# Optimization experiments

Hardware: AMD Instinct MI355X
Metric: run time of the kernel (lower is better)

Reference implementation:

```python
import jax, jax.numpy as jnp
import numpy as np

B, S, D, H = 4, 4096, 512, 512


def setup_inputs() -> dict:
    key = jax.random.key(0)
    ks = jax.random.split(key, 11)
    def rn(k, shape):
        return jax.random.normal(k, shape, dtype=jnp.float32)
    return {
        "query": rn(ks[0], (B, 1, D)),
        "keys": rn(ks[1], (B, S, D)),
        "values": rn(ks[2], (B, S, D)),
        "Wq": rn(ks[3], (D, H)) / np.sqrt(D),
        "bq": rn(ks[4], (H,)) * 0.02,
        "Wk": rn(ks[5], (D, H)) / np.sqrt(D),
        "bk": rn(ks[6], (H,)) * 0.02,
        "Wv": rn(ks[7], (D, H)) / np.sqrt(D),
        "bv": rn(ks[8], (H,)) * 0.02,
        "Wo": rn(ks[9], (H, D)) / np.sqrt(H),
        "bo": rn(ks[10], (D,)) * 0.02,
    }


def reference(query, keys, values, Wq, bq, Wk, bk, Wv, bv, Wo, bo):
    # projections
    q = query @ Wq + bq      # (B, 1, H)
    k = keys @ Wk + bk       # (B, S, H)
    v = values @ Wv + bv     # (B, S, H)
    scale = jnp.sqrt(jnp.asarray(q.shape[-1], dtype=jnp.float32))
    # single-query scores: (B, 1, S)
    scores = jnp.einsum('bqh,bsh->bqs', q, k)
    seq = k.shape[1]
    # torch masked_fill broadcasts (B,1,S) against tril (1,S,S) -> (B,S,S)
    causal = jnp.tril(jnp.ones((seq, seq), dtype=bool))[None]  # (1, S, S)
    masked = jnp.where(causal, scores, -jnp.inf)                # (B, S, S)
    attn_weights = jax.nn.softmax(masked / scale, axis=-1)      # (B, S, S)
    context = jnp.einsum('brs,bsh->brh', attn_weights, v)       # (B, S, H)
    out = context @ Wo + bo                                     # (B, S, D)
    return out, attn_weights
```

## Files before the change

kernel.cpp:

```cpp
#include <hip/hip_runtime.h>
#include <hip/hip_bf16.h>

#define BB 4
#define SS 4096
#define DD 512
#define HH 512

typedef __attribute__((ext_vector_type(8))) short bf16x8;
typedef __attribute__((ext_vector_type(4))) float f32x4;

__global__ __launch_bounds__(256) void k_pre1(const float* __restrict__ query,
                                              const float* __restrict__ Wq,
                                              const float* __restrict__ bq,
                                              const float* __restrict__ Wv,
                                              const float* __restrict__ Wo,
                                              float* __restrict__ qv,
                                              float* __restrict__ Wvop) {
    __shared__ float smem[8320];
    int wb = blockIdx.x, tid = threadIdx.x;
    if (wb < 32) {
        float* qs = smem;
        float (*red)[64] = reinterpret_cast<float(*)[64]>(smem + 512);
        int hg = wb & 7, b = wb >> 3;
        int hl = tid & 63, qq = tid >> 6;
        int h = hg * 64 + hl;
        for (int d = tid; d < DD; d += 256) qs[d] = query[b * DD + d];
        __syncthreads();
        float a = 0.f;
        int d0 = qq * 128;
        for (int d = d0; d < d0 + 128; ++d)
            a += qs[d] * Wq[(size_t)d * HH + h];
        red[qq][hl] = a;
        __syncthreads();
        if (tid < 64)
            qv[b * HH + hg * 64 + tid] = red[0][tid] + red[1][tid] + red[2][tid] + red[3][tid]
                                       + bq[hg * 64 + tid];
    } else {
        int t = wb - 32;
        int hs = t >> 6, rem = t & 63;
        int n0 = (rem & 7) * 64, k0 = (rem >> 3) * 64;
        float (*lo)[65] = reinterpret_cast<float(*)[65]>(smem);
        float (*lv)[65] = reinterpret_cast<float(*)[65]>(smem + 4160);
        int tn = (tid & 15) * 4, tk = (tid >> 4) * 4;
        float acc[4][4] = {};
        int hbase = hs * 128;
        for (int h0 = hbase; h0 < hbase + 128; h0 += 64) {
            for (int i = tid; i < 64 * 64; i += 256) {
                int rr = i >> 6, cc = i & 63;
                lo[rr][cc] = Wo[(size_t)(h0 + rr) * DD + n0 + cc];
                lv[rr][cc] = Wv[(size_t)(k0 + rr) * HH + h0 + cc];
            }
            __syncthreads();
            for (int h = 0; h < 64; ++h)
#pragma unroll
                for (int a = 0; a < 4; ++a) {
                    float vv = lv[tk + a][h];
#pragma unroll
                    for (int c = 0; c < 4; ++c) acc[a][c] += vv * lo[h][tn + c];
                }
            __syncthreads();
        }
        float* dst = Wvop + (size_t)hs * (DD * HH);
        for (int a = 0; a < 4; ++a)
            for (int c = 0; c < 4; ++c)
                dst[(size_t)(k0 + tk + a) * DD + n0 + tn + c] = acc[a][c];
    }
}

__global__ __launch_bounds__(256) void k_pre2(const float* __restrict__ Wk,
                                              const float* __restrict__ qv,
                                              const float* __restrict__ bk,
                                              const float* __restrict__ Wvop,
                                              const float* __restrict__ bv,
                                              const float* __restrict__ Wo,
                                              const float* __restrict__ bo,
                                              float* __restrict__ wout,
                                              float* __restrict__ cq,
                                              __hip_bfloat16* __restrict__ WvoT,
                                              float* __restrict__ bfinal) {
    __shared__ float smem[4160];
    int wb = blockIdx.x, tid = threadIdx.x;
    if (wb < 512) {
        float* qs = smem;
        float* red = smem + 512;
        int b = wb >> 7, dg = wb & 127;
        int wid = tid >> 6, lane = tid & 63;
        for (int h = tid; h < HH; h += 256) qs[h] = qv[b * HH + h];
        __syncthreads();
        int d = dg * 4 + wid;
        const float4* row = reinterpret_cast<const float4*>(Wk + (size_t)d * HH);
        float4 r0 = row[lane * 2], r1 = row[lane * 2 + 1];
        int h = lane * 8;
        float acc = r0.x * qs[h] + r0.y * qs[h + 1] + r0.z * qs[h + 2] + r0.w * qs[h + 3]
                  + r1.x * qs[h + 4] + r1.y * qs[h + 5] + r1.z * qs[h + 6] + r1.w * qs[h + 7];
        for (int off = 32; off > 0; off >>= 1) acc += __shfl_down(acc, off);
        if (lane == 0) wout[b * DD + d] = acc;
        if (dg == 0) {
            red[tid] = qs[tid] * bk[tid] + qs[tid + 256] * bk[tid + 256];
            __syncthreads();
            for (int off = 128; off > 0; off >>= 1) {
                if (tid < off) red[tid] += red[tid + off];
                __syncthreads();
            }
            if (tid == 0) cq[b] = red[0];
        }
    } else if (wb < 576) {
        int t = wb - 512;
        int n0 = (t & 7) * 64, k0 = (t >> 3) * 64;
        float (*ts)[65] = reinterpret_cast<float(*)[65]>(smem);
#pragma unroll
        for (int i = 0; i < 16; ++i) {
            int idx = tid + i * 256;
            int kk = idx >> 6, nn = idx & 63;
            size_t off = (size_t)(k0 + kk) * DD + n0 + nn;
            float s = Wvop[off] + Wvop[(size_t)DD * HH + off]
                    + Wvop[2 * (size_t)DD * HH + off] + Wvop[3 * (size_t)DD * HH + off];
            ts[nn][kk] = s;
        }
        __syncthreads();
#pragma unroll
        for (int i = 0; i < 16; ++i) {
            int idx = tid + i * 256;
            int row = idx >> 6, col = idx & 63;
            WvoT[(size_t)(n0 + row) * DD + k0 + col] = __float2bfloat16(ts[row][col]);
        }
    } else {
        int n0 = (wb - 576) * 64;
        int nn = tid & 63, hs = tid >> 6;
        float acc = 0.f;
        for (int hh = 0; hh < 128; ++hh) {
            int h = hs * 128 + hh;
            acc += bv[h] * Wo[(size_t)h * DD + n0 + nn];
        }
        float (*red)[64] = reinterpret_cast<float(*)[64]>(smem);
        red[hs][nn] = acc;
        __syncthreads();
        if (tid < 64)
            bfinal[n0 + tid] = red[0][tid] + red[1][tid] + red[2][tid] + red[3][tid]
                             + bo[n0 + tid];
    }
}

__global__ __launch_bounds__(256) void k_scores(const float* __restrict__ keys,
                                                const float* __restrict__ wv,
                                                const float* __restrict__ cq,
                                                float* __restrict__ scores) {
    __shared__ float ws[DD];
    int wb = blockIdx.x, tid = threadIdx.x;
    int b = wb >> 10, sg = wb & 1023;
    int wid = tid >> 6, lane = tid & 63;
    for (int d = tid; d < DD; d += 256) ws[d] = wv[b * DD + d];
    __syncthreads();
    int s = sg * 4 + wid;
    const float4* row = reinterpret_cast<const float4*>(keys + ((size_t)b * SS + s) * DD);
    float4 r0 = row[lane * 2], r1 = row[lane * 2 + 1];
    int h = lane * 8;
    float acc = r0.x * ws[h] + r0.y * ws[h + 1] + r0.z * ws[h + 2] + r0.w * ws[h + 3]
              + r1.x * ws[h + 4] + r1.y * ws[h + 5] + r1.z * ws[h + 6] + r1.w * ws[h + 7];
    for (int off = 32; off > 0; off >>= 1) acc += __shfl_down(acc, off);
    if (lane == 0) scores[b * SS + s] = acc + cq[b];
}

__global__ __launch_bounds__(1024) void k_softmax(const float* __restrict__ scores,
                                                  float* __restrict__ p,
                                                  float* __restrict__ inv_cum) {
    int b = blockIdx.x, tid = threadIdx.x;
    int wid = tid >> 6, lane = tid & 63;
    __shared__ float wmax[16];
    __shared__ float wsum[16];
    const float inv_scale = 0.04419417382415922f;
    float4 sv = *reinterpret_cast<const float4*>(scores + (size_t)b * SS + tid * 4);
    float loc[4] = {sv.x * inv_scale, sv.y * inv_scale, sv.z * inv_scale, sv.w * inv_scale};
    float mx = fmaxf(fmaxf(loc[0], loc[1]), fmaxf(loc[2], loc[3]));
    for (int off = 32; off > 0; off >>= 1) mx = fmaxf(mx, __shfl_xor(mx, off));
    if (lane == 0) wmax[wid] = mx;
    __syncthreads();
    float M = wmax[0];
    for (int i = 1; i < 16; ++i) M = fmaxf(M, wmax[i]);
    float own = 0.f;
    for (int j = 0; j < 4; ++j) {
        loc[j] = expf(loc[j] - M);
        own += loc[j];
    }
    float incl = own;
    for (int off = 1; off < 64; off <<= 1) {
        float v = __shfl_up(incl, off);
        if (lane >= off) incl += v;
    }
    if (lane == 63) wsum[wid] = incl;
    __syncthreads();
    float woff = 0.f;
    for (int i = 0; i < wid; ++i) woff += wsum[i];
    float run = woff + incl - own;
    float4 pv, iv;
    run += loc[0]; pv.x = loc[0]; iv.x = 1.f / run;
    run += loc[1]; pv.y = loc[1]; iv.y = 1.f / run;
    run += loc[2]; pv.z = loc[2]; iv.z = 1.f / run;
    run += loc[3]; pv.w = loc[3]; iv.w = 1.f / run;
    *reinterpret_cast<float4*>(p + (size_t)b * SS + tid * 4) = pv;
    *reinterpret_cast<float4*>(inv_cum + (size_t)b * SS + tid * 4) = iv;
}

__global__ void k_tile(const float* __restrict__ values, const float* __restrict__ p,
                       float* __restrict__ T64) {
    int chunk = blockIdx.x, t = blockIdx.y, b = blockIdx.z, tid = threadIdx.x;
    __shared__ float ps[64];
    ps[tid] = p[b * SS + t * 64 + tid];
    __syncthreads();
    int d = chunk * 256 + tid * 4;
    const float* vp = values + ((size_t)b * SS + (size_t)t * 64) * DD + d;
    f32x4 acc = {0.f, 0.f, 0.f, 0.f};
    for (int i = 0; i < 64; ++i) {
        float4 v = *reinterpret_cast<const float4*>(vp + (size_t)i * DD);
        float pi = ps[i];
        acc[0] += pi * v.x; acc[1] += pi * v.y; acc[2] += pi * v.z; acc[3] += pi * v.w;
    }
    *reinterpret_cast<f32x4*>(&T64[((size_t)b * 64 + t) * DD + d]) = acc;
}

__global__ __launch_bounds__(512) void k_fat(const float* __restrict__ values,
                                             const float* __restrict__ p,
                                             const float* __restrict__ icum,
                                             const float* __restrict__ T64,
                                             const __hip_bfloat16* __restrict__ Bt,
                                             const float* __restrict__ bfinal,
                                             float* __restrict__ Out,
                                             float* __restrict__ attn) {
    __shared__ __align__(16) short As[64][512];
    __shared__ float ps[64], ics[64];
    int bx = blockIdx.x, tid = threadIdx.x;
    if (bx < 256) {
        int b = bx >> 6, tb = bx & 63;
        int m0 = bx * 64;
        if (tid < 64) ps[tid] = p[b * SS + tb * 64 + tid];
        else if (tid < 128) ics[tid - 64] = icum[b * SS + tb * 64 + (tid - 64)];
        float acc = 0.f;
        for (int t = 0; t < tb; ++t) acc += T64[((size_t)b * 64 + t) * DD + tid];
        __syncthreads();
        const float* vp = values + ((size_t)b * SS + (size_t)tb * 64) * DD + tid;
        int gcol = tid >> 3, gsub = tid & 7;
        for (int i = 0; i < 64; ++i) {
            acc += ps[i] * vp[(size_t)i * DD];
            __hip_bfloat16 cv = __float2bfloat16(acc * ics[i]);
            short sv;
            __builtin_memcpy(&sv, &cv, 2);
            As[i][(((gcol ^ (i & 7)) << 3) | gsub)] = sv;
        }
        __syncthreads();
        int wv = tid >> 6, lane = tid & 63;
        int n0 = wv * 64;
        int lrow = lane & 15, lk = (lane >> 4) * 8;
        f32x4 oacc[4][4] = {};
        const short* Bp = reinterpret_cast<const short*>(Bt);
        for (int kk = 0; kk < 512; kk += 32) {
            int gbase = (kk + lk) >> 3;
            bf16x8 af[4], bfr[4];
#pragma unroll
            for (int i = 0; i < 4; ++i) {
                int row = i * 16 + lrow;
                af[i] = *reinterpret_cast<const bf16x8*>(&As[row][((gbase ^ (row & 7)) << 3)]);
            }
#pragma unroll
            for (int j = 0; j < 4; ++j)
                bfr[j] = *reinterpret_cast<const bf16x8*>(Bp + (size_t)(n0 + j * 16 + lrow) * 512 + kk + lk);
#pragma unroll
            for (int i = 0; i < 4; ++i)
#pragma unroll
                for (int j = 0; j < 4; ++j)
                    oacc[i][j] = __builtin_amdgcn_mfma_f32_16x16x32_bf16(af[i], bfr[j], oacc[i][j], 0, 0, 0);
        }
        int rbase = (lane >> 4) * 4;
        for (int i = 0; i < 4; ++i)
            for (int j = 0; j < 4; ++j) {
                int col = n0 + j * 16 + lrow;
                float bb = bfinal[col];
#pragma unroll
                for (int r = 0; r < 4; ++r) {
                    int row = m0 + i * 16 + rbase + r;
                    Out[(size_t)row * DD + col] = oacc[i][j][r] + bb;
                }
            }
    } else {
        int ab = bx - 256;
        int b = ab >> 9, rblk = ab & 511;
        int r0 = rblk * 8;
        const float* pb = p + b * SS;
        float4 pv[2];
        pv[0] = *reinterpret_cast<const float4*>(pb + tid * 4);
        pv[1] = *reinterpret_cast<const float4*>(pb + 2048 + tid * 4);
        const float* icb = icum + b * SS + r0;
#pragma unroll
        for (int row = 0; row < 8; ++row) {
            int r = r0 + row;
            float ic = icb[row];
            size_t base = ((size_t)b * SS + r) * SS;
#pragma unroll
            for (int g = 0; g < 2; ++g) {
                int s = g * 2048 + tid * 4;
                float4 o;
                o.x = (s + 0 <= r) ? pv[g].x * ic : 0.f;
                o.y = (s + 1 <= r) ? pv[g].y * ic : 0.f;
                o.z = (s + 2 <= r) ? pv[g].z * ic : 0.f;
                o.w = (s + 3 <= r) ? pv[g].w * ic : 0.f;
                *reinterpret_cast<float4*>(&attn[base + s]) = o;
            }
        }
    }
}

extern "C" void kernel_launch(void* const* d_in, const int* in_sizes, int n_in,
                              void* d_out, int out_size, void* d_ws, size_t ws_size,
                              hipStream_t stream) {
    const float* query  = (const float*)d_in[0];
    const float* keys   = (const float*)d_in[1];
    const float* values = (const float*)d_in[2];
    const float* Wq = (const float*)d_in[3];
    const float* bq = (const float*)d_in[4];
    const float* Wk = (const float*)d_in[5];
    const float* bk = (const float*)d_in[6];
    const float* Wv = (const float*)d_in[7];
    const float* bv = (const float*)d_in[8];
    const float* Wo = (const float*)d_in[9];
    const float* bo = (const float*)d_in[10];

    float* out  = (float*)d_out;
    float* attn = out + (size_t)BB * SS * DD;

    char* ws = (char*)d_ws;
    float* Wvop = (float*)(ws);
    __hip_bfloat16* WvoT = (__hip_bfloat16*)(ws + 4194304);
    float* T64  = (float*)(ws + 4718592);
    float* p    = (float*)(ws + 5242880);
    float* icum = (float*)(ws + 5308416);
    float* scr  = (float*)(ws + 5373952);
    float* qv   = (float*)(ws + 5439488);
    float* wv   = (float*)(ws + 5447680);
    float* cq   = (float*)(ws + 5455872);
    float* bfin = (float*)(ws + 5456128);

    k_pre1   <<<288,              256, 0, stream>>>(query, Wq, bq, Wv, Wo, qv, Wvop);
    k_pre2   <<<584,              256, 0, stream>>>(Wk, qv, bk, Wvop, bv, Wo, bo,
                                                    wv, cq, WvoT, bfin);
    k_scores <<<4096,             256, 0, stream>>>(keys, wv, cq, scr);
    k_softmax<<<BB,              1024, 0, stream>>>(scr, p, icum);
    k_tile   <<<dim3(2, 64, BB),   64, 0, stream>>>(values, p, T64);
    k_fat    <<<2304,             512, 0, stream>>>(values, p, icum, T64, WvoT, bfin,
                                                    out, attn);
}
```

Baseline: 118.6 us.

## Split attn-weight writes across tile and fat kernels to fill tile-kernel idle time

```diff
diff --git a/kernel.cpp b/kernel.cpp
--- a/kernel.cpp
+++ b/kernel.cpp
@@ -201,31 +201,57 @@
     *reinterpret_cast<float4*>(inv_cum + (size_t)b * SS + tid * 4) = iv;
 }
 
-__global__ void k_tile(const float* __restrict__ values, const float* __restrict__ p,
-                       float* __restrict__ T64) {
-    int chunk = blockIdx.x, t = blockIdx.y, b = blockIdx.z, tid = threadIdx.x;
+__global__ __launch_bounds__(512) void k_tail1(const float* __restrict__ values,
+                                               const float* __restrict__ p,
+                                               const float* __restrict__ icum,
+                                               float* __restrict__ T64,
+                                               float* __restrict__ attn) {
     __shared__ float ps[64];
-    ps[tid] = p[b * SS + t * 64 + tid];
-    __syncthreads();
-    int d = chunk * 256 + tid * 4;
-    const float* vp = values + ((size_t)b * SS + (size_t)t * 64) * DD + d;
-    f32x4 acc = {0.f, 0.f, 0.f, 0.f};
-    for (int i = 0; i < 64; ++i) {
-        float4 v = *reinterpret_cast<const float4*>(vp + (size_t)i * DD);
-        float pi = ps[i];
-        acc[0] += pi * v.x; acc[1] += pi * v.y; acc[2] += pi * v.z; acc[3] += pi * v.w;
-    }
-    *reinterpret_cast<f32x4*>(&T64[((size_t)b * 64 + t) * DD + d]) = acc;
-}
-
-__global__ __launch_bounds__(512) void k_fat(const float* __restrict__ values,
-                                             const float* __restrict__ p,
-                                             const float* __restrict__ icum,
-                                             const float* __restrict__ T64,
-                                             const __hip_bfloat16* __restrict__ Bt,
-                                             const float* __restrict__ bfinal,
-                                             float* __restrict__ Out,
-                                             float* __restrict__ attn) {
+    int bx = blockIdx.x, tid = threadIdx.x;
+    if (bx < 256) {
+        int b = bx >> 6, t = bx & 63;
+        if (tid < 64) ps[tid] = p[b * SS + t * 64 + tid];
+        __syncthreads();
+        const float* vp = values + ((size_t)b * SS + (size_t)t * 64) * DD + tid;
+        float acc = 0.f;
+        for (int i = 0; i < 64; ++i) acc += ps[i] * vp[(size_t)i * DD];
+        T64[((size_t)b * 64 + t) * DD + tid] = acc;
+    } else {
+        int u = bx - 256;
+        int b = u & 3, rblk = u >> 2;
+        int r0 = rblk * 8;
+        const float* pb = p + b * SS;
+        float4 pv[2];
+        pv[0] = *reinterpret_cast<const float4*>(pb + tid * 4);
+        pv[1] = *reinterpret_cast<const float4*>(pb + 2048 + tid * 4);
+        const float* icb = icum + b * SS + r0;
+#pragma unroll
+        for (int row = 0; row < 8; ++row) {
+            int r = r0 + row;
+            float ic = icb[row];
+            size_t base = ((size_t)b * SS + r) * SS;
+#pragma unroll
+            for (int g = 0; g < 2; ++g) {
+                int s = g * 2048 + tid * 4;
+                float4 o;
+                o.x = (s + 0 <= r) ? pv[g].x * ic : 0.f;
+                o.y = (s + 1 <= r) ? pv[g].y * ic : 0.f;
+                o.z = (s + 2 <= r) ? pv[g].z * ic : 0.f;
+                o.w = (s + 3 <= r) ? pv[g].w * ic : 0.f;
+                *reinterpret_cast<float4*>(&attn[base + s]) = o;
+            }
+        }
+    }
+}
+
+__global__ __launch_bounds__(512) void k_tail2(const float* __restrict__ values,
+                                               const float* __restrict__ p,
+                                               const float* __restrict__ icum,
+                                               const float* __restrict__ T64,
+                                               const __hip_bfloat16* __restrict__ Bt,
+                                               const float* __restrict__ bfinal,
+                                               float* __restrict__ Out,
+                                               float* __restrict__ attn) {
     __shared__ __align__(16) short As[64][512];
     __shared__ float ps[64], ics[64];
     int bx = blockIdx.x, tid = threadIdx.x;
@@ -281,8 +307,8 @@
                 }
             }
     } else {
-        int ab = bx - 256;
-        int b = ab >> 9, rblk = ab & 511;
+        int u = bx - 256;
+        int b = u & 3, rblk = 288 + (u >> 2);
         int r0 = rblk * 8;
         const float* pb = p + b * SS;
         float4 pv[2];
@@ -338,12 +364,10 @@
     float* cq   = (float*)(ws + 5455872);
     float* bfin = (float*)(ws + 5456128);
 
-    k_pre1   <<<288,              256, 0, stream>>>(query, Wq, bq, Wv, Wo, qv, Wvop);
-    k_pre2   <<<584,              256, 0, stream>>>(Wk, qv, bk, Wvop, bv, Wo, bo,
-                                                    wv, cq, WvoT, bfin);
-    k_scores <<<4096,             256, 0, stream>>>(keys, wv, cq, scr);
-    k_softmax<<<BB,              1024, 0, stream>>>(scr, p, icum);
-    k_tile   <<<dim3(2, 64, BB),   64, 0, stream>>>(values, p, T64);
-    k_fat    <<<2304,             512, 0, stream>>>(values, p, icum, T64, WvoT, bfin,
-                                                    out, attn);
-}
+    k_pre1   <<<288,   256, 0, stream>>>(query, Wq, bq, Wv, Wo, qv, Wvop);
+    k_pre2   <<<584,   256, 0, stream>>>(Wk, qv, bk, Wvop, bv, Wo, bo, wv, cq, WvoT, bfin);
+    k_scores <<<4096,  256, 0, stream>>>(keys, wv, cq, scr);
+    k_softmax<<<BB,   1024, 0, stream>>>(scr, p, icum);
+    k_tail1  <<<1408,  512, 0, stream>>>(values, p, icum, T64, attn);
+    k_tail2  <<<1152,  512, 0, stream>>>(values, p, icum, T64, WvoT, bfin, out, attn);
+}
```

Measured after the change: 131.1 us. 10.5% more time.

## Fuse softmax into scores kernel via last-block atomic counter per batch

Applied to the files above, without the earlier changes.

```diff
diff --git a/kernel.cpp b/kernel.cpp
--- a/kernel.cpp
+++ b/kernel.cpp
@@ -141,44 +141,56 @@
     }
 }
 
-__global__ __launch_bounds__(256) void k_scores(const float* __restrict__ keys,
-                                                const float* __restrict__ wv,
-                                                const float* __restrict__ cq,
-                                                float* __restrict__ scores) {
-    __shared__ float ws[DD];
+__global__ __launch_bounds__(256) void k_scores_sm(const float* __restrict__ keys,
+                                                   const float* __restrict__ wv,
+                                                   const float* __restrict__ cq,
+                                                   float* __restrict__ scores,
+                                                   float* __restrict__ p,
+                                                   float* __restrict__ inv_cum,
+                                                   unsigned int* __restrict__ cnt) {
+    __shared__ float smem[512];
+    __shared__ unsigned int sflag;
     int wb = blockIdx.x, tid = threadIdx.x;
     int b = wb >> 10, sg = wb & 1023;
     int wid = tid >> 6, lane = tid & 63;
-    for (int d = tid; d < DD; d += 256) ws[d] = wv[b * DD + d];
+    for (int d = tid; d < DD; d += 256) smem[d] = wv[b * DD + d];
     __syncthreads();
     int s = sg * 4 + wid;
-    const float4* row = reinterpret_cast<const float4*>(keys + ((size_t)b * SS + s) * DD);
-    float4 r0 = row[lane * 2], r1 = row[lane * 2 + 1];
-    int h = lane * 8;
-    float acc = r0.x * ws[h] + r0.y * ws[h + 1] + r0.z * ws[h + 2] + r0.w * ws[h + 3]
-              + r1.x * ws[h + 4] + r1.y * ws[h + 5] + r1.z * ws[h + 6] + r1.w * ws[h + 7];
-    for (int off = 32; off > 0; off >>= 1) acc += __shfl_down(acc, off);
-    if (lane == 0) scores[b * SS + s] = acc + cq[b];
-}
-
-__global__ __launch_bounds__(1024) void k_softmax(const float* __restrict__ scores,
-                                                  float* __restrict__ p,
-                                                  float* __restrict__ inv_cum) {
-    int b = blockIdx.x, tid = threadIdx.x;
-    int wid = tid >> 6, lane = tid & 63;
-    __shared__ float wmax[16];
-    __shared__ float wsum[16];
+    {
+        const float4* row = reinterpret_cast<const float4*>(keys + ((size_t)b * SS + s) * DD);
+        float4 r0 = row[lane * 2], r1 = row[lane * 2 + 1];
+        int h = lane * 8;
+        float acc = r0.x * smem[h] + r0.y * smem[h + 1] + r0.z * smem[h + 2] + r0.w * smem[h + 3]
+                  + r1.x * smem[h + 4] + r1.y * smem[h + 5] + r1.z * smem[h + 6] + r1.w * smem[h + 7];
+        for (int off = 32; off > 0; off >>= 1) acc += __shfl_down(acc, off);
+        if (lane == 0) scores[b * SS + s] = acc + cq[b];
+    }
+    __threadfence();
+    __syncthreads();
+    if (tid == 0) sflag = atomicAdd(&cnt[b], 1u);
+    __syncthreads();
+    if (sflag != 1023u) return;
+    __threadfence();
     const float inv_scale = 0.04419417382415922f;
-    float4 sv = *reinterpret_cast<const float4*>(scores + (size_t)b * SS + tid * 4);
-    float loc[4] = {sv.x * inv_scale, sv.y * inv_scale, sv.z * inv_scale, sv.w * inv_scale};
-    float mx = fmaxf(fmaxf(loc[0], loc[1]), fmaxf(loc[2], loc[3]));
+    const float* sb = scores + (size_t)b * SS;
+    float loc[16];
+    float mx = -1e30f;
+#pragma unroll
+    for (int g = 0; g < 4; ++g) {
+        float4 sv = *reinterpret_cast<const float4*>(sb + tid * 16 + g * 4);
+        loc[g * 4 + 0] = sv.x * inv_scale; loc[g * 4 + 1] = sv.y * inv_scale;
+        loc[g * 4 + 2] = sv.z * inv_scale; loc[g * 4 + 3] = sv.w * inv_scale;
+        mx = fmaxf(mx, fmaxf(fmaxf(loc[g * 4], loc[g * 4 + 1]),
+                             fmaxf(loc[g * 4 + 2], loc[g * 4 + 3])));
+    }
     for (int off = 32; off > 0; off >>= 1) mx = fmaxf(mx, __shfl_xor(mx, off));
-    if (lane == 0) wmax[wid] = mx;
-    __syncthreads();
-    float M = wmax[0];
-    for (int i = 1; i < 16; ++i) M = fmaxf(M, wmax[i]);
+    __syncthreads();
+    if (lane == 0) smem[wid] = mx;
+    __syncthreads();
+    float M = fmaxf(fmaxf(smem[0], smem[1]), fmaxf(smem[2], smem[3]));
     float own = 0.f;
-    for (int j = 0; j < 4; ++j) {
+#pragma unroll
+    for (int j = 0; j < 16; ++j) {
         loc[j] = expf(loc[j] - M);
         own += loc[j];
     }
@@ -187,18 +199,23 @@
         float v = __shfl_up(incl, off);
         if (lane >= off) incl += v;
     }
-    if (lane == 63) wsum[wid] = incl;
+    if (lane == 63) smem[8 + wid] = incl;
     __syncthreads();
     float woff = 0.f;
-    for (int i = 0; i < wid; ++i) woff += wsum[i];
+    for (int i = 0; i < wid; ++i) woff += smem[8 + i];
     float run = woff + incl - own;
-    float4 pv, iv;
-    run += loc[0]; pv.x = loc[0]; iv.x = 1.f / run;
-    run += loc[1]; pv.y = loc[1]; iv.y = 1.f / run;
-    run += loc[2]; pv.z = loc[2]; iv.z = 1.f / run;
-    run += loc[3]; pv.w = loc[3]; iv.w = 1.f / run;
-    *reinterpret_cast<float4*>(p + (size_t)b * SS + tid * 4) = pv;
-    *reinterpret_cast<float4*>(inv_cum + (size_t)b * SS + tid * 4) = iv;
+    float* pb = p + (size_t)b * SS + tid * 16;
+    float* ib = inv_cum + (size_t)b * SS + tid * 16;
+#pragma unroll
+    for (int g = 0; g < 4; ++g) {
+        float4 pv4, iv4;
+        run += loc[g * 4 + 0]; pv4.x = loc[g * 4 + 0]; iv4.x = 1.f / run;
+        run += loc[g * 4 + 1]; pv4.y = loc[g * 4 + 1]; iv4.y = 1.f / run;
+        run += loc[g * 4 + 2]; pv4.z = loc[g * 4 + 2]; iv4.z = 1.f / run;
+        run += loc[g * 4 + 3]; pv4.w = loc[g * 4 + 3]; iv4.w = 1.f / run;
+        *reinterpret_cast<float4*>(pb + g * 4) = pv4;
+        *reinterpret_cast<float4*>(ib + g * 4) = iv4;
+    }
 }
 
 __global__ void k_tile(const float* __restrict__ values, const float* __restrict__ p,
@@ -337,13 +354,14 @@
     float* wv   = (float*)(ws + 5447680);
     float* cq   = (float*)(ws + 5455872);
     float* bfin = (float*)(ws + 5456128);
-
-    k_pre1   <<<288,              256, 0, stream>>>(query, Wq, bq, Wv, Wo, qv, Wvop);
-    k_pre2   <<<584,              256, 0, stream>>>(Wk, qv, bk, Wvop, bv, Wo, bo,
-                                                    wv, cq, WvoT, bfin);
-    k_scores <<<4096,             256, 0, stream>>>(keys, wv, cq, scr);
-    k_softmax<<<BB,              1024, 0, stream>>>(scr, p, icum);
-    k_tile   <<<dim3(2, 64, BB),   64, 0, stream>>>(values, p, T64);
-    k_fat    <<<2304,             512, 0, stream>>>(values, p, icum, T64, WvoT, bfin,
-                                                    out, attn);
-}
+    unsigned int* cnt = (unsigned int*)(ws + 5458176);
+
+    hipMemsetAsync(cnt, 0, 4 * sizeof(unsigned int), stream);
+    k_pre1     <<<288,             256, 0, stream>>>(query, Wq, bq, Wv, Wo, qv, Wvop);
+    k_pre2     <<<584,             256, 0, stream>>>(Wk, qv, bk, Wvop, bv, Wo, bo,
+                                                     wv, cq, WvoT, bfin);
+    k_scores_sm<<<4096,            256, 0, stream>>>(keys, wv, cq, scr, p, icum, cnt);
+    k_tile     <<<dim3(2, 64, BB),  64, 0, stream>>>(values, p, T64);
+    k_fat      <<<2304,            512, 0, stream>>>(values, p, icum, T64, WvoT, bfin,
+                                                     out, attn);
+}
```

After: 435.9 us. +267.6%, slower.

## Fold exp into score kernel and merge cumulative scan with tile reduction

Applied to the files above, without the earlier changes.

```diff
diff --git a/kernel.cpp b/kernel.cpp
--- a/kernel.cpp
+++ b/kernel.cpp
@@ -141,10 +141,10 @@
     }
 }
 
-__global__ __launch_bounds__(256) void k_scores(const float* __restrict__ keys,
-                                                const float* __restrict__ wv,
-                                                const float* __restrict__ cq,
-                                                float* __restrict__ scores) {
+__global__ __launch_bounds__(256) void k_scores_p(const float* __restrict__ keys,
+                                                  const float* __restrict__ wv,
+                                                  const float* __restrict__ cq,
+                                                  float* __restrict__ p) {
     __shared__ float ws[DD];
     int wb = blockIdx.x, tid = threadIdx.x;
     int b = wb >> 10, sg = wb & 1023;
@@ -158,64 +158,58 @@
     float acc = r0.x * ws[h] + r0.y * ws[h + 1] + r0.z * ws[h + 2] + r0.w * ws[h + 3]
               + r1.x * ws[h + 4] + r1.y * ws[h + 5] + r1.z * ws[h + 6] + r1.w * ws[h + 7];
     for (int off = 32; off > 0; off >>= 1) acc += __shfl_down(acc, off);
-    if (lane == 0) scores[b * SS + s] = acc + cq[b];
-}
-
-__global__ __launch_bounds__(1024) void k_softmax(const float* __restrict__ scores,
-                                                  float* __restrict__ p,
+    const float inv_scale = 0.04419417382415922f;
+    if (lane == 0) p[b * SS + s] = expf((acc + cq[b]) * inv_scale);
+}
+
+__global__ __launch_bounds__(64) void k_tile_scan(const float* __restrict__ values,
+                                                  const float* __restrict__ p,
+                                                  float* __restrict__ T64,
                                                   float* __restrict__ inv_cum) {
-    int b = blockIdx.x, tid = threadIdx.x;
-    int wid = tid >> 6, lane = tid & 63;
-    __shared__ float wmax[16];
-    __shared__ float wsum[16];
-    const float inv_scale = 0.04419417382415922f;
-    float4 sv = *reinterpret_cast<const float4*>(scores + (size_t)b * SS + tid * 4);
-    float loc[4] = {sv.x * inv_scale, sv.y * inv_scale, sv.z * inv_scale, sv.w * inv_scale};
-    float mx = fmaxf(fmaxf(loc[0], loc[1]), fmaxf(loc[2], loc[3]));
-    for (int off = 32; off > 0; off >>= 1) mx = fmaxf(mx, __shfl_xor(mx, off));
-    if (lane == 0) wmax[wid] = mx;
-    __syncthreads();
-    float M = wmax[0];
-    for (int i = 1; i < 16; ++i) M = fmaxf(M, wmax[i]);
-    float own = 0.f;
-    for (int j = 0; j < 4; ++j) {
-        loc[j] = expf(loc[j] - M);
-        own += loc[j];
+    int bx = blockIdx.x, tid = threadIdx.x;
+    if (bx < 512) {
+        __shared__ float ps[64];
+        int b = bx >> 7, t = (bx >> 1) & 63, chunk = bx & 1;
+        ps[tid] = p[b * SS + t * 64 + tid];
+        __syncthreads();
+        int d = chunk * 256 + tid * 4;
+        const float* vp = values + ((size_t)b * SS + (size_t)t * 64) * DD + d;
+        f32x4 acc = {0.f, 0.f, 0.f, 0.f};
+        for (int i = 0; i < 64; ++i) {
+            float4 v = *reinterpret_cast<const float4*>(vp + (size_t)i * DD);
+            float pi = ps[i];
+            acc[0] += pi * v.x; acc[1] += pi * v.y; acc[2] += pi * v.z; acc[3] += pi * v.w;
+        }
+        *reinterpret_cast<f32x4*>(&T64[((size_t)b * 64 + t) * DD + d]) = acc;
+    } else {
+        int b = bx - 512;
+        const float* pb = p + (size_t)b * SS;
+        float loc[64];
+        float own = 0.f;
+#pragma unroll
+        for (int g = 0; g < 16; ++g) {
+            float4 v = *reinterpret_cast<const float4*>(pb + tid * 64 + g * 4);
+            loc[g * 4 + 0] = v.x; loc[g * 4 + 1] = v.y;
+            loc[g * 4 + 2] = v.z; loc[g * 4 + 3] = v.w;
+            own += v.x + v.y + v.z + v.w;
+        }
+        float incl = own;
+        for (int off = 1; off < 64; off <<= 1) {
+            float v = __shfl_up(incl, off);
+            if (tid >= off) incl += v;
+        }
+        float run = incl - own;
+        float* ib = inv_cum + (size_t)b * SS + tid * 64;
+#pragma unroll
+        for (int g = 0; g < 16; ++g) {
+            float4 iv;
+            run += loc[g * 4 + 0]; iv.x = 1.f / run;
+            run += loc[g * 4 + 1]; iv.y = 1.f / run;
+            run += loc[g * 4 + 2]; iv.z = 1.f / run;
+            run += loc[g * 4 + 3]; iv.w = 1.f / run;
+            *reinterpret_cast<float4*>(ib + g * 4) = iv;
+        }
     }
-    float incl = own;
-    for (int off = 1; off < 64; off <<= 1) {
-        float v = __shfl_up(incl, off);
-        if (lane >= off) incl += v;
-    }
-    if (lane == 63) wsum[wid] = incl;
-    __syncthreads();
-    float woff = 0.f;
-    for (int i = 0; i < wid; ++i) woff += wsum[i];
-    float run = woff + incl - own;
-    float4 pv, iv;
-    run += loc[0]; pv.x = loc[0]; iv.x = 1.f / run;
-    run += loc[1]; pv.y = loc[1]; iv.y = 1.f / run;
-    run += loc[2]; pv.z = loc[2]; iv.z = 1.f / run;
-    run += loc[3]; pv.w = loc[3]; iv.w = 1.f / run;
-    *reinterpret_cast<float4*>(p + (size_t)b * SS + tid * 4) = pv;
-    *reinterpret_cast<float4*>(inv_cum + (size_t)b * SS + tid * 4) = iv;
-}
-
-__global__ void k_tile(const float* __restrict__ values, const float* __restrict__ p,
-                       float* __restrict__ T64) {
-    int chunk = blockIdx.x, t = blockIdx.y, b = blockIdx.z, tid = threadIdx.x;
-    __shared__ float ps[64];
-    ps[tid] = p[b * SS + t * 64 + tid];
-    __syncthreads();
-    int d = chunk * 256 + tid * 4;
-    const float* vp = values + ((size_t)b * SS + (size_t)t * 64) * DD + d;
-    f32x4 acc = {0.f, 0.f, 0.f, 0.f};
-    for (int i = 0; i < 64; ++i) {
-        float4 v = *reinterpret_cast<const float4*>(vp + (size_t)i * DD);
-        float pi = ps[i];
-        acc[0] += pi * v.x; acc[1] += pi * v.y; acc[2] += pi * v.z; acc[3] += pi * v.w;
-    }
-    *reinterpret_cast<f32x4*>(&T64[((size_t)b * 64 + t) * DD + d]) = acc;
 }
 
 __global__ __launch_bounds__(512) void k_fat(const float* __restrict__ values,
@@ -332,18 +326,14 @@
     float* T64  = (float*)(ws + 4718592);
     float* p    = (float*)(ws + 5242880);
     float* icum = (float*)(ws + 5308416);
-    float* scr  = (float*)(ws + 5373952);
-    float* qv   = (float*)(ws + 5439488);
-    float* wv   = (float*)(ws + 5447680);
-    float* cq   = (float*)(ws + 5455872);
-    float* bfin = (float*)(ws + 5456128);
-
-    k_pre1   <<<288,              256, 0, stream>>>(query, Wq, bq, Wv, Wo, qv, Wvop);
-    k_pre2   <<<584,              256, 0, stream>>>(Wk, qv, bk, Wvop, bv, Wo, bo,
-                                                    wv, cq, WvoT, bfin);
-    k_scores <<<4096,             256, 0, stream>>>(keys, wv, cq, scr);
-    k_softmax<<<BB,              1024, 0, stream>>>(scr, p, icum);
-    k_tile   <<<dim3(2, 64, BB),   64, 0, stream>>>(values, p, T64);
-    k_fat    <<<2304,             512, 0, stream>>>(values, p, icum, T64, WvoT, bfin,
-                                                    out, attn);
-}
+    float* qv   = (float*)(ws + 5373952);
+    float* wv   = (float*)(ws + 5382144);
+    float* cq   = (float*)(ws + 5390336);
+    float* bfin = (float*)(ws + 5390592);
+
+    k_pre1     <<<288,   256, 0, stream>>>(query, Wq, bq, Wv, Wo, qv, Wvop);
+    k_pre2     <<<584,   256, 0, stream>>>(Wk, qv, bk, Wvop, bv, Wo, bo, wv, cq, WvoT, bfin);
+    k_scores_p <<<4096,  256, 0, stream>>>(keys, wv, cq, p);
+    k_tile_scan<<<516,    64, 0, stream>>>(values, p, T64, icum);
+    k_fat      <<<2304,  512, 0, stream>>>(values, p, icum, T64, WvoT, bfin, out, attn);
+}
```

Result: faster. 115.2 us, median of 2 (-2.9%).
